# Performance work log

Measured on AMD Instinct MI355X. Metric: run time of the kernel, lower is better.

## Reference

```python
import jax, jax.numpy as jnp
import numpy as np

DIM_QK = 1024


def setup_inputs() -> dict:
    key = jax.random.key(0)
    ks = jax.random.split(key, 5)
    B, S, D = 4, 2048, 1024
    return {
        "x": jax.random.normal(ks[0], (B, S, D), dtype=jnp.float32),
        "Wq": jax.random.normal(ks[1], (DIM_QK, D), dtype=jnp.float32) * (D ** -0.5),
        "Wk": jax.random.normal(ks[2], (DIM_QK, D), dtype=jnp.float32) * (D ** -0.5),
        "Wv": jax.random.normal(ks[3], (D, D), dtype=jnp.float32) * (D ** -0.5),
        "Wo": jax.random.normal(ks[4], (D, D), dtype=jnp.float32) * (D ** -0.5),
    }


def reference(x, Wq, Wk, Wv, Wo):
    # torch Linear: y = x @ W.T (no bias)
    q = jnp.einsum('bsd,kd->bsk', x, Wq)
    k = jnp.einsum('bsd,kd->bsk', x, Wk)
    v = jnp.einsum('bsd,vd->bsv', x, Wv)
    scale = (DIM_QK // 2) ** (-0.5)
    dist = jnp.einsum('bqk,btk->bqt', q, k) * scale  # [B,S,S]
    weight = jax.lax.stop_gradient(dist)             # pre-softmax scores (detached)
    attn = jax.nn.softmax(dist, axis=-1)
    ctx = jnp.einsum('bqt,btv->bqv', attn, v)
    out = jnp.einsum('bqv,ev->bqe', ctx, Wo)
    return (out, weight)
```

## Files before the change

kernel.cpp:

```cpp
#include <hip/hip_runtime.h>
#include <stdint.h>

typedef __attribute__((ext_vector_type(8))) short bf16x8;
typedef __attribute__((ext_vector_type(4))) float f32x4;

__device__ __forceinline__ unsigned short f32_to_bf16(float f) {
  union { float f; unsigned int u; } v; v.f = f;
  unsigned int u = v.u;
  u += 0x7fffu + ((u >> 16) & 1u);
  return (unsigned short)(u >> 16);
}

__device__ __forceinline__ void gload_lds16(const unsigned short* g, unsigned short* lds_p) {
  __builtin_amdgcn_global_load_lds(
      (const __attribute__((address_space(1))) unsigned int*)g,
      (__attribute__((address_space(3))) unsigned int*)lds_p,
      16, 0, 0);
}


#define VM8  asm volatile("s_waitcnt vmcnt(8)" ::: "memory")
#define VM6  asm volatile("s_waitcnt vmcnt(6)" ::: "memory")
#define VM4  asm volatile("s_waitcnt vmcnt(4)" ::: "memory")
#define VM3  asm volatile("s_waitcnt vmcnt(3)" ::: "memory")
#define VM0_ asm volatile("s_waitcnt vmcnt(0)" ::: "memory")
#define VMNO ((void)0)


#define ISSUE_A(KT, KK) do {                                                  \
    const unsigned short* ga_ = As0 + (KT) * 64 + (KK) * 32;                  \
    unsigned short* la_ = &lds[(((KT) & 1) << 15) + (KK) * 8192 + t * 8];     \
    gload_lds16(ga_, la_);                                                    \
    gload_lds16(ga_ + a128, la_ + 4096);                                      \
  } while (0)

#define ISSUE_B(KT, KK) do {                                                  \
    const unsigned short* gb_ = Bs0 + (KT) * 64 + (KK) * 32;                  \
    unsigned short* lb_ = &lds[(((KT) & 1) << 15) + 16384 + (KK) * 8192 + t * 8]; \
    gload_lds16(gb_, lb_);                                                    \
    gload_lds16(gb_ + b128, lb_ + 4096);                                      \
  } while (0)

#define PH(BUFB, KK, MH, LOADB, ISSUE_CODE, VMC) do {                         \
    const int ab_ = (BUFB) + (KK) * 8192;                                     \
    if (LOADB) {                                                              \
      const int bb2_ = (BUFB) + 16384 + (KK) * 8192;                          \
      _Pragma("unroll")                                                       \
      for (int ni_ = 0; ni_ < 4; ++ni_)                                       \
        bfr[ni_] = *(const bf16x8*)&lds[bb2_ + (wc + ni_ * 16 + lrow) * 32 + q8s]; \
    }                                                                         \
    bf16x8 af_[4];                                                            \
    _Pragma("unroll")                                                         \
    for (int mi_ = 0; mi_ < 4; ++mi_)                                         \
      af_[mi_] = *(const bf16x8*)&lds[ab_ + (wr + (MH) * 64 + mi_ * 16 + lrow) * 32 + q8s]; \
    ISSUE_CODE;                                                               \
    __builtin_amdgcn_s_setprio(1);                                            \
    _Pragma("unroll")                                                         \
    for (int mi_ = 0; mi_ < 4; ++mi_) {                                       \
      _Pragma("unroll")                                                       \
      for (int ni_ = 0; ni_ < 4; ++ni_)                                       \
        acc[(MH) * 4 + mi_][ni_] = __builtin_amdgcn_mfma_f32_16x16x32_bf16(   \
            af_[mi_], bfr[ni_], acc[(MH) * 4 + mi_][ni_], 0, 0, 0);           \
    }                                                                         \
    __builtin_amdgcn_s_setprio(0);                                            \
    VMC;                                                                      \
    asm volatile("s_waitcnt lgkmcnt(0)" ::: "memory");                        \
    __builtin_amdgcn_s_barrier();                                             \
    asm volatile("" ::: "memory");                                            \
  } while (0)

template<int MODE>
__global__ __launch_bounds__(512, 2)
void gemm_bt(const unsigned short* __restrict__ A,
             const unsigned short* __restrict__ Bm,
             void* __restrict__ Cv,
             int M, int N, int K, int lda, int ldb, int ldc,
             long sA_, long sB_, long sC_,
             float scale)
{
  __shared__ unsigned short lds[65536];

  const int bz = blockIdx.z;
  const unsigned short* Ab = A + (long)bz * sA_;
  const unsigned short* Bb = Bm + (long)bz * sB_;

  const int m0 = blockIdx.x * 256;
  const int n0 = blockIdx.y * 256;

  const int t = threadIdx.x;
  const int lane = t & 63;
  const int w = t >> 6;
  const int wr = (w >> 2) * 128;
  const int wc = (w & 3) * 64;
  const int lrow = lane & 15;
  const int q8s = (((lane >> 4) ^ ((lrow >> 1) & 3)) * 8);

  const int row0 = t >> 2;
  const int kc0 = (((t & 3) ^ ((t >> 3) & 3)) * 8);
  const unsigned short* As0 = Ab + (long)(m0 + row0) * lda + kc0;
  const unsigned short* Bs0 = Bb + (long)(n0 + row0) * ldb + kc0;
  const long a128 = (long)lda * 128;
  const long b128 = (long)ldb * 128;

  f32x4 acc[8][4];
#pragma unroll
  for (int i = 0; i < 8; ++i)
#pragma unroll
    for (int j = 0; j < 4; ++j)
      acc[i][j] = (f32x4){0.f, 0.f, 0.f, 0.f};

  const int NT = K >> 6;

  ISSUE_A(0, 0); ISSUE_B(0, 0);
  ISSUE_A(0, 1); ISSUE_B(0, 1);
  ISSUE_A(1, 0); ISSUE_B(1, 0);
  VM8;
  __builtin_amdgcn_s_barrier();
  asm volatile("" ::: "memory");

  bf16x8 bfr[4];
  int kt = 0;
  for (; kt < NT - 2; ++kt) {
    const int bb = (kt & 1) << 15;
    PH(bb, 0, 0, 1, ISSUE_A(kt + 1, 1), VMNO);
    PH(bb, 0, 1, 0, ISSUE_B(kt + 1, 1), VM8);
    PH(bb, 1, 0, 1, ISSUE_A(kt + 2, 0), VMNO);
    PH(bb, 1, 1, 0, ISSUE_B(kt + 2, 0), VM8);
  }
  {
    const int bb = (kt & 1) << 15;
    PH(bb, 0, 0, 1, ISSUE_A(kt + 1, 1), VMNO);
    PH(bb, 0, 1, 0, ISSUE_B(kt + 1, 1), VM8);
    PH(bb, 1, 0, 1, VMNO, VMNO);
    PH(bb, 1, 1, 0, VMNO, VM4);
    ++kt;
  }
  {
    const int bb = (kt & 1) << 15;
    PH(bb, 0, 0, 1, VMNO, VMNO);
    PH(bb, 0, 1, 0, VMNO, VM0_);
    PH(bb, 1, 0, 1, VMNO, VMNO);
    PH(bb, 1, 1, 0, VMNO, VMNO);
  }

  const int cl = lane & 15;
  const int rq = (lane >> 4) * 4;

  if (MODE == 2) {
    float* Cb = (float*)Cv + (long)bz * sC_;
#pragma unroll
    for (int mig = 0; mig < 8; ++mig) {
      const int rowb = m0 + wr + (mig >> 2) * 64 + (mig & 3) * 16 + rq;
#pragma unroll
      for (int ni = 0; ni < 4; ++ni) {
        const int col = n0 + wc + ni * 16 + cl;
#pragma unroll
        for (int r = 0; r < 4; ++r)
          Cb[(long)(rowb + r) * ldc + col] = acc[mig][ni][r] * scale;
      }
    }
  } else {
    unsigned short* Cb = (unsigned short*)Cv + (long)bz * sC_;
#pragma unroll
    for (int mig = 0; mig < 8; ++mig) {
      const int rowb = m0 + wr + (mig >> 2) * 64 + (mig & 3) * 16 + rq;
#pragma unroll
      for (int ni = 0; ni < 4; ++ni) {
        const int col = n0 + wc + ni * 16 + cl;
#pragma unroll
        for (int r = 0; r < 4; ++r)
          Cb[(long)(rowb + r) * ldc + col] = f32_to_bf16(acc[mig][ni][r]);
      }
    }
  }
}


#define ISSUE_A1(KT, KK) do {                                                 \
    gload_lds16(As0 + (KT) * 64 + (KK) * 32,                                  \
                &lds[((KT) & 1) * 24576 + (KK) * 4096 + t * 8]);              \
  } while (0)

#define ISSUE_B1(KT, KK) do {                                                 \
    const unsigned short* gb_ = Bs0 + (KT) * 64 + (KK) * 32;                  \
    unsigned short* lb_ = &lds[((KT) & 1) * 24576 + 8192 + (KK) * 8192 + t * 8]; \
    gload_lds16(gb_, lb_);                                                    \
    gload_lds16(gb_ + b128, lb_ + 4096);                                      \
  } while (0)

#define PH2(BUFB, KK, ISSUE_CODE, VMC) do {                                   \
    const int ab_ = (BUFB) + (KK) * 4096;                                     \
    const int bb_ = (BUFB) + 8192 + (KK) * 8192;                              \
    bf16x8 af_[4], bf_[4];                                                    \
    _Pragma("unroll")                                                         \
    for (int i_ = 0; i_ < 4; ++i_) {                                          \
      af_[i_] = *(const bf16x8*)&lds[ab_ + (wr + i_ * 16 + lrow) * 32 + q8s]; \
      bf_[i_] = *(const bf16x8*)&lds[bb_ + (wc + i_ * 16 + lrow) * 32 + q8s]; \
    }                                                                         \
    ISSUE_CODE;                                                               \
    __builtin_amdgcn_s_setprio(1);                                            \
    _Pragma("unroll")                                                         \
    for (int mi_ = 0; mi_ < 4; ++mi_) {                                       \
      _Pragma("unroll")                                                       \
      for (int ni_ = 0; ni_ < 4; ++ni_)                                       \
        acc[mi_][ni_] = __builtin_amdgcn_mfma_f32_16x16x32_bf16(              \
            af_[mi_], bf_[ni_], acc[mi_][ni_], 0, 0, 0);                      \
    }                                                                         \
    __builtin_amdgcn_s_setprio(0);                                            \
    VMC;                                                                      \
    asm volatile("s_waitcnt lgkmcnt(0)" ::: "memory");                        \
    __builtin_amdgcn_s_barrier();                                             \
    asm volatile("" ::: "memory");                                            \
  } while (0)

template<int MODE>
__global__ __launch_bounds__(512, 2)
void gemm_bt_128(const unsigned short* __restrict__ A,
                 const unsigned short* __restrict__ Bm,
                 void* __restrict__ Cv,
                 int M, int N, int K, int lda, int ldb, int ldc,
                 long sA_, long sB_, long sC_,
                 float scale)
{
  __shared__ unsigned short lds[49152];

  const int bz = blockIdx.z;
  const unsigned short* Ab = A + (long)bz * sA_;
  const unsigned short* Bb = Bm + (long)bz * sB_;

  const int m0 = blockIdx.x * 128;
  const int n0 = blockIdx.y * 256;

  const int t = threadIdx.x;
  const int lane = t & 63;
  const int w = t >> 6;
  const int wr = (w >> 2) * 64;
  const int wc = (w & 3) * 64;
  const int lrow = lane & 15;
  const int q8s = (((lane >> 4) ^ ((lrow >> 1) & 3)) * 8);

  const int row0 = t >> 2;
  const int kc0 = (((t & 3) ^ ((t >> 3) & 3)) * 8);
  const unsigned short* As0 = Ab + (long)(m0 + row0) * lda + kc0;
  const unsigned short* Bs0 = Bb + (long)(n0 + row0) * ldb + kc0;
  const long b128 = (long)ldb * 128;

  f32x4 acc[4][4];
#pragma unroll
  for (int i = 0; i < 4; ++i)
#pragma unroll
    for (int j = 0; j < 4; ++j)
      acc[i][j] = (f32x4){0.f, 0.f, 0.f, 0.f};

  const int NT = K >> 6;

  ISSUE_A1(0, 0); ISSUE_B1(0, 0);
  ISSUE_A1(0, 1); ISSUE_B1(0, 1);
  ISSUE_A1(1, 0); ISSUE_B1(1, 0);
  VM6;
  __builtin_amdgcn_s_barrier();
  asm volatile("" ::: "memory");

  int kt = 0;
  for (; kt < NT - 2; ++kt) {
    const int bb = (kt & 1) * 24576;
    PH2(bb, 0, { ISSUE_A1(kt + 1, 1); ISSUE_B1(kt + 1, 1); }, VM6);
    PH2(bb, 1, { ISSUE_A1(kt + 2, 0); ISSUE_B1(kt + 2, 0); }, VM6);
  }
  {
    const int bb = (kt & 1) * 24576;
    PH2(bb, 0, { ISSUE_A1(kt + 1, 1); ISSUE_B1(kt + 1, 1); }, VM6);
    PH2(bb, 1, {}, VM3);
    ++kt;
  }
  {
    const int bb = (kt & 1) * 24576;
    PH2(bb, 0, {}, VM0_);
    PH2(bb, 1, {}, VMNO);
  }

  const int cl = lane & 15;
  const int rq = (lane >> 4) * 4;

  if (MODE == 2) {
    float* Cb = (float*)Cv + (long)bz * sC_;
#pragma unroll
    for (int mi = 0; mi < 4; ++mi) {
      const int rowb = m0 + wr + mi * 16 + rq;
#pragma unroll
      for (int ni = 0; ni < 4; ++ni) {
        const int col = n0 + wc + ni * 16 + cl;
#pragma unroll
        for (int r = 0; r < 4; ++r)
          Cb[(long)(rowb + r) * ldc + col] = acc[mi][ni][r] * scale;
      }
    }
  } else {
    unsigned short* Cb = (unsigned short*)Cv + (long)bz * sC_;
#pragma unroll
    for (int mi = 0; mi < 4; ++mi) {
      const int rowb = m0 + wr + mi * 16 + rq;
#pragma unroll
      for (int ni = 0; ni < 4; ++ni) {
        const int col = n0 + wc + ni * 16 + cl;
#pragma unroll
        for (int r = 0; r < 4; ++r)
          Cb[(long)(rowb + r) * ldc + col] = f32_to_bf16(acc[mi][ni][r]);
      }
    }
  }
}

__global__ __launch_bounds__(256)
void softmax_rows(const float* __restrict__ dist, unsigned short* __restrict__ attn) {
  const long row = blockIdx.x;
  const float4* in = (const float4*)(dist + row * 2048);
  const int t = threadIdx.x;
  float4 v0 = in[t];
  float4 v1 = in[t + 256];

  float m = fmaxf(fmaxf(fmaxf(v0.x, v0.y), fmaxf(v0.z, v0.w)),
                  fmaxf(fmaxf(v1.x, v1.y), fmaxf(v1.z, v1.w)));
#pragma unroll
  for (int off = 32; off > 0; off >>= 1)
    m = fmaxf(m, __shfl_xor(m, off, 64));

  __shared__ float redm[4];
  __shared__ float reds[4];
  if ((t & 63) == 0) redm[t >> 6] = m;
  __syncthreads();
  m = fmaxf(fmaxf(redm[0], redm[1]), fmaxf(redm[2], redm[3]));

  float e[8];
  e[0] = __expf(v0.x - m); e[1] = __expf(v0.y - m);
  e[2] = __expf(v0.z - m); e[3] = __expf(v0.w - m);
  e[4] = __expf(v1.x - m); e[5] = __expf(v1.y - m);
  e[6] = __expf(v1.z - m); e[7] = __expf(v1.w - m);

  float s = ((e[0] + e[1]) + (e[2] + e[3])) + ((e[4] + e[5]) + (e[6] + e[7]));
#pragma unroll
  for (int off = 32; off > 0; off >>= 1)
    s += __shfl_xor(s, off, 64);
  if ((t & 63) == 0) reds[t >> 6] = s;
  __syncthreads();
  s = (reds[0] + reds[1]) + (reds[2] + reds[3]);

  const float inv = 1.0f / s;
  ushort4 o0, o1;
  o0.x = f32_to_bf16(e[0] * inv); o0.y = f32_to_bf16(e[1] * inv);
  o0.z = f32_to_bf16(e[2] * inv); o0.w = f32_to_bf16(e[3] * inv);
  o1.x = f32_to_bf16(e[4] * inv); o1.y = f32_to_bf16(e[5] * inv);
  o1.z = f32_to_bf16(e[6] * inv); o1.w = f32_to_bf16(e[7] * inv);
  *(ushort4*)(attn + row * 2048 + t * 4) = o0;
  *(ushort4*)(attn + row * 2048 + 1024 + t * 4) = o1;
}

__global__ __launch_bounds__(256)
void cast_all(const float* __restrict__ Wq, const float* __restrict__ Wk,
              const float* __restrict__ Wv, const float* __restrict__ Wo,
              const float* __restrict__ x, unsigned short* __restrict__ dst) {
  const long i = ((long)blockIdx.x * 256 + threadIdx.x) * 4;
  const float* src;
  long off;
  if (i < 4194304) {
    const int which = (int)(i >> 20);
    src = (which == 0) ? Wq : (which == 1) ? Wk : (which == 2) ? Wv : Wo;
    off = i & 1048575;
  } else {
    src = x;
    off = i - 4194304;
  }
  float4 v = *(const float4*)(src + off);
  ushort4 o;
  o.x = f32_to_bf16(v.x); o.y = f32_to_bf16(v.y);
  o.z = f32_to_bf16(v.z); o.w = f32_to_bf16(v.w);
  *(ushort4*)(dst + i) = o;
}

extern "C" void kernel_launch(void* const* d_in, const int* in_sizes, int n_in,
                              void* d_out, int out_size, void* d_ws, size_t ws_size,
                              hipStream_t stream) {
  const float* x  = (const float*)d_in[0];
  const float* Wq = (const float*)d_in[1];
  const float* Wk = (const float*)d_in[2];
  const float* Wv = (const float*)d_in[3];
  const float* Wo = (const float*)d_in[4];

  const long Bn = 4, S = 2048, D = 1024;
  const long MS = Bn * S;

  float* out_p  = (float*)d_out;
  float* weight = out_p + MS * D;

  unsigned short* Wqb = (unsigned short*)d_ws;
  unsigned short* Wvb = Wqb + 2 * D * D;
  unsigned short* Wob = Wvb + D * D;
  unsigned short* xb  = Wob + D * D;
  unsigned short* qk  = xb + MS * D;
  unsigned short* vtb = qk + MS * 2048;
  unsigned short* attn = qk;
  unsigned short* ctx  = xb;

  cast_all<<<12288, 256, 0, stream>>>(Wq, Wk, Wv, Wo, x, Wqb);

  gemm_bt<0><<<dim3(32, 8, 1), 512, 0, stream>>>(xb, Wqb, qk, 8192, 2048, 1024,
                                                 1024, 1024, 2048, 0, 0, 0, 1.f);
  gemm_bt_128<0><<<dim3(8, 8, 4), 512, 0, stream>>>(Wvb, xb, vtb, 1024, 2048, 1024,
                                                    1024, 1024, 2048, 0, S * D, D * S, 1.f);
  gemm_bt<2><<<dim3(8, 8, 4), 512, 0, stream>>>(qk, qk + 1024, weight, 2048, 2048, 1024,
                                                2048, 2048, 2048,
                                                S * 2048, S * 2048, S * S,
                                                0.04419417382415922f);
  softmax_rows<<<(int)(Bn * S), 256, 0, stream>>>(weight, attn);
  gemm_bt_128<0><<<dim3(16, 4, 4), 512, 0, stream>>>(attn, vtb, ctx, 2048, 1024, 2048,
                                                     2048, 2048, 1024,
                                                     S * S, D * S, S * D, 1.f);
  gemm_bt_128<2><<<dim3(64, 4, 1), 512, 0, stream>>>(ctx, Wob, out_p, 8192, 1024, 1024,
                                                     1024, 1024, 1024, 0, 0, 0, 1.f);
}
```

Measured before the change: 308.1 us.

## Restructure GEMM pipelines: barrier before MFMA, triple-buffer 128 kernel, flatten V^T layout

The waitcnt and barrier now sit before the MFMA block in both GEMM kernels, so each phase waits for its loads and then computes, with a trailing barrier after. The 256-row kernel drops to a one-tile-ahead prefetch that fills the other half of its double buffer. The 128-row kernel moves to a three-stage LDS ring (larger shared array), prefetching two tiles ahead with rotating read and write offsets. The V^T projection now runs as one flat GEMM over all batches, writing an [D, B*S] layout, and the attn@V GEMM uses the matching stride. The larger LDS footprint may reduce occupancy, and the shallower prefetch in the 256-row kernel may expose more memory latency.

```diff
diff --git a/kernel.cpp b/kernel.cpp
--- a/kernel.cpp
+++ b/kernel.cpp
@@ -19,12 +19,13 @@
 }
 
 
-#define VM8  asm volatile("s_waitcnt vmcnt(8)" ::: "memory")
+#define VM9  asm volatile("s_waitcnt vmcnt(9)" ::: "memory")
 #define VM6  asm volatile("s_waitcnt vmcnt(6)" ::: "memory")
 #define VM4  asm volatile("s_waitcnt vmcnt(4)" ::: "memory")
 #define VM3  asm volatile("s_waitcnt vmcnt(3)" ::: "memory")
 #define VM0_ asm volatile("s_waitcnt vmcnt(0)" ::: "memory")
 #define VMNO ((void)0)
+#define FENCE asm volatile("" ::: "memory")
 
 
 #define ISSUE_A(KT, KK) do {                                                  \
@@ -54,6 +55,10 @@
     for (int mi_ = 0; mi_ < 4; ++mi_)                                         \
       af_[mi_] = *(const bf16x8*)&lds[ab_ + (wr + (MH) * 64 + mi_ * 16 + lrow) * 32 + q8s]; \
     ISSUE_CODE;                                                               \
+    VMC;                                                                      \
+    FENCE;                                                                    \
+    __builtin_amdgcn_s_barrier();                                             \
+    asm volatile("s_waitcnt lgkmcnt(0)" ::: "memory");                        \
     __builtin_amdgcn_s_setprio(1);                                            \
     _Pragma("unroll")                                                         \
     for (int mi_ = 0; mi_ < 4; ++mi_) {                                       \
@@ -63,10 +68,9 @@
             af_[mi_], bfr[ni_], acc[(MH) * 4 + mi_][ni_], 0, 0, 0);           \
     }                                                                         \
     __builtin_amdgcn_s_setprio(0);                                            \
-    VMC;                                                                      \
-    asm volatile("s_waitcnt lgkmcnt(0)" ::: "memory");                        \
+    FENCE;                                                                    \
     __builtin_amdgcn_s_barrier();                                             \
-    asm volatile("" ::: "memory");                                            \
+    FENCE;                                                                    \
   } while (0)
 
 template<int MODE>
@@ -113,27 +117,19 @@
 
   ISSUE_A(0, 0); ISSUE_B(0, 0);
   ISSUE_A(0, 1); ISSUE_B(0, 1);
-  ISSUE_A(1, 0); ISSUE_B(1, 0);
-  VM8;
+  VM4;
+  FENCE;
   __builtin_amdgcn_s_barrier();
-  asm volatile("" ::: "memory");
+  FENCE;
 
   bf16x8 bfr[4];
   int kt = 0;
-  for (; kt < NT - 2; ++kt) {
+  for (; kt < NT - 1; ++kt) {
     const int bb = (kt & 1) << 15;
-    PH(bb, 0, 0, 1, ISSUE_A(kt + 1, 1), VMNO);
-    PH(bb, 0, 1, 0, ISSUE_B(kt + 1, 1), VM8);
-    PH(bb, 1, 0, 1, ISSUE_A(kt + 2, 0), VMNO);
-    PH(bb, 1, 1, 0, ISSUE_B(kt + 2, 0), VM8);
-  }
-  {
-    const int bb = (kt & 1) << 15;
-    PH(bb, 0, 0, 1, ISSUE_A(kt + 1, 1), VMNO);
-    PH(bb, 0, 1, 0, ISSUE_B(kt + 1, 1), VM8);
-    PH(bb, 1, 0, 1, VMNO, VMNO);
-    PH(bb, 1, 1, 0, VMNO, VM4);
-    ++kt;
+    PH(bb, 0, 0, 1, ISSUE_A(kt + 1, 0), VMNO);
+    PH(bb, 0, 1, 0, ISSUE_B(kt + 1, 0), VM4);
+    PH(bb, 1, 0, 1, ISSUE_A(kt + 1, 1), VMNO);
+    PH(bb, 1, 1, 0, ISSUE_B(kt + 1, 1), VM4);
   }
   {
     const int bb = (kt & 1) << 15;
@@ -176,21 +172,17 @@
 }
 
 
-#define ISSUE_A1(KT, KK) do {                                                 \
-    gload_lds16(As0 + (KT) * 64 + (KK) * 32,                                  \
-                &lds[((KT) & 1) * 24576 + (KK) * 4096 + t * 8]);              \
-  } while (0)
-
-#define ISSUE_B1(KT, KK) do {                                                 \
-    const unsigned short* gb_ = Bs0 + (KT) * 64 + (KK) * 32;                  \
-    unsigned short* lb_ = &lds[((KT) & 1) * 24576 + 8192 + (KK) * 8192 + t * 8]; \
+#define ISSUE3(GK, KK, WB) do {                                               \
+    gload_lds16(As0 + (GK) + (KK) * 32, &lds[(WB) + (KK) * 4096 + t * 8]);    \
+    const unsigned short* gb_ = Bs0 + (GK) + (KK) * 32;                       \
+    unsigned short* lb_ = &lds[(WB) + 8192 + (KK) * 8192 + t * 8];            \
     gload_lds16(gb_, lb_);                                                    \
     gload_lds16(gb_ + b128, lb_ + 4096);                                      \
   } while (0)
 
-#define PH2(BUFB, KK, ISSUE_CODE, VMC) do {                                   \
-    const int ab_ = (BUFB) + (KK) * 4096;                                     \
-    const int bb_ = (BUFB) + 8192 + (KK) * 8192;                              \
+#define PH2(RB, KK, ISSUE_CODE, VMC) do {                                     \
+    const int ab_ = (RB) + (KK) * 4096;                                       \
+    const int bb_ = (RB) + 8192 + (KK) * 8192;                                \
     bf16x8 af_[4], bf_[4];                                                    \
     _Pragma("unroll")                                                         \
     for (int i_ = 0; i_ < 4; ++i_) {                                          \
@@ -198,6 +190,10 @@
       bf_[i_] = *(const bf16x8*)&lds[bb_ + (wc + i_ * 16 + lrow) * 32 + q8s]; \
     }                                                                         \
     ISSUE_CODE;                                                               \
+    VMC;                                                                      \
+    FENCE;                                                                    \
+    __builtin_amdgcn_s_barrier();                                             \
+    asm volatile("s_waitcnt lgkmcnt(0)" ::: "memory");                        \
     __builtin_amdgcn_s_setprio(1);                                            \
     _Pragma("unroll")                                                         \
     for (int mi_ = 0; mi_ < 4; ++mi_) {                                       \
@@ -207,10 +203,9 @@
             af_[mi_], bf_[ni_], acc[mi_][ni_], 0, 0, 0);                      \
     }                                                                         \
     __builtin_amdgcn_s_setprio(0);                                            \
-    VMC;                                                                      \
-    asm volatile("s_waitcnt lgkmcnt(0)" ::: "memory");                        \
+    FENCE;                                                                    \
     __builtin_amdgcn_s_barrier();                                             \
-    asm volatile("" ::: "memory");                                            \
+    FENCE;                                                                    \
   } while (0)
 
 template<int MODE>
@@ -222,7 +217,7 @@
                  long sA_, long sB_, long sC_,
                  float scale)
 {
-  __shared__ unsigned short lds[49152];
+  __shared__ unsigned short lds[73728];
 
   const int bz = blockIdx.z;
   const unsigned short* Ab = A + (long)bz * sA_;
@@ -254,29 +249,31 @@
 
   const int NT = K >> 6;
 
-  ISSUE_A1(0, 0); ISSUE_B1(0, 0);
-  ISSUE_A1(0, 1); ISSUE_B1(0, 1);
-  ISSUE_A1(1, 0); ISSUE_B1(1, 0);
-  VM6;
+  ISSUE3(0, 0, 0);  ISSUE3(0, 1, 0);
+  ISSUE3(64, 0, 24576); ISSUE3(64, 1, 24576);
+  VM9;
+  FENCE;
   __builtin_amdgcn_s_barrier();
-  asm volatile("" ::: "memory");
-
+  FENCE;
+
+  int rb = 0;
+  int wb = 49152;
   int kt = 0;
   for (; kt < NT - 2; ++kt) {
-    const int bb = (kt & 1) * 24576;
-    PH2(bb, 0, { ISSUE_A1(kt + 1, 1); ISSUE_B1(kt + 1, 1); }, VM6);
-    PH2(bb, 1, { ISSUE_A1(kt + 2, 0); ISSUE_B1(kt + 2, 0); }, VM6);
+    const int gk = (kt + 2) * 64;
+    PH2(rb, 0, ISSUE3(gk, 0, wb), VM9);
+    PH2(rb, 1, ISSUE3(gk, 1, wb), VM9);
+    rb = (rb == 49152) ? 0 : rb + 24576;
+    wb = (wb == 49152) ? 0 : wb + 24576;
   }
   {
-    const int bb = (kt & 1) * 24576;
-    PH2(bb, 0, { ISSUE_A1(kt + 1, 1); ISSUE_B1(kt + 1, 1); }, VM6);
-    PH2(bb, 1, {}, VM3);
-    ++kt;
+    PH2(rb, 0, VMNO, VM6);
+    PH2(rb, 1, VMNO, VM3);
+    rb = (rb == 49152) ? 0 : rb + 24576;
   }
   {
-    const int bb = (kt & 1) * 24576;
-    PH2(bb, 0, {}, VM0_);
-    PH2(bb, 1, {}, VMNO);
+    PH2(rb, 0, VMNO, VM0_);
+    PH2(rb, 1, VMNO, VMNO);
   }
 
   const int cl = lane & 15;
@@ -405,16 +402,16 @@
 
   gemm_bt<0><<<dim3(32, 8, 1), 512, 0, stream>>>(xb, Wqb, qk, 8192, 2048, 1024,
                                                  1024, 1024, 2048, 0, 0, 0, 1.f);
-  gemm_bt_128<0><<<dim3(8, 8, 4), 512, 0, stream>>>(Wvb, xb, vtb, 1024, 2048, 1024,
-                                                    1024, 1024, 2048, 0, S * D, D * S, 1.f);
+  gemm_bt_128<0><<<dim3(8, 32, 1), 512, 0, stream>>>(Wvb, xb, vtb, 1024, 8192, 1024,
+                                                     1024, 1024, 8192, 0, 0, 0, 1.f);
   gemm_bt<2><<<dim3(8, 8, 4), 512, 0, stream>>>(qk, qk + 1024, weight, 2048, 2048, 1024,
                                                 2048, 2048, 2048,
                                                 S * 2048, S * 2048, S * S,
                                                 0.04419417382415922f);
   softmax_rows<<<(int)(Bn * S), 256, 0, stream>>>(weight, attn);
   gemm_bt_128<0><<<dim3(16, 4, 4), 512, 0, stream>>>(attn, vtb, ctx, 2048, 1024, 2048,
-                                                     2048, 2048, 1024,
-                                                     S * S, D * S, S * D, 1.f);
+                                                     2048, 8192, 1024,
+                                                     S * S, 2048, S * D, 1.f);
   gemm_bt_128<2><<<dim3(64, 4, 1), 512, 0, stream>>>(ctx, Wob, out_p, 8192, 1024, 1024,
                                                      1024, 1024, 1024, 0, 0, 0, 1.f);
 }
```

Measured after the change: 312.5 us. No clear change (+1.4%).
